# Kernel tuning notes

Hardware: AMD Instinct MI355X
Metric: run time of the kernel (lower is better)

## Reference

```python
import jax, jax.numpy as jnp
import numpy as np

N = 50000      # nodes
E = 800000     # edges (avg degree 16)
F_IN = 256
F_OUT = 128
ALPHA = 0.2    # leaky-relu negative slope


def setup_inputs() -> dict:
    key = jax.random.key(0)
    k1, k2, k3, k4 = jax.random.split(key, 4)
    x = jax.random.normal(k1, (N, F_IN), dtype=jnp.float32)
    # xavier_uniform-like scale for W (gain=1.414)
    limit_w = 1.414 * np.sqrt(6.0 / (F_IN + F_OUT))
    W = jax.random.uniform(k2, (F_IN, F_OUT), dtype=jnp.float32, minval=-limit_w, maxval=limit_w)
    limit_a = 1.414 * np.sqrt(6.0 / (2 * F_OUT + 1))
    a = jax.random.uniform(k3, (2 * F_OUT, 1), dtype=jnp.float32, minval=-limit_a, maxval=limit_a)
    edge = jax.random.randint(k4, (2, E), 0, N)  # edge[0]=row/src, edge[1]=col/dst
    return {"x": x, "W": W, "a": a, "edge": edge}


def reference(x, W, a, edge):
    h = x @ W                                   # [N, F_OUT]
    src, dst = edge[0], edge[1]                 # [E], [E]
    # cat([h_i, h_j], 1) @ a == h_i @ a[:F] + h_j @ a[F:] -> compute per-node halves once
    s_src = h @ a[:F_OUT, 0]                    # [N]
    s_dst = h @ a[F_OUT:, 0]                    # [N]
    e = jax.nn.leaky_relu(s_src[src] + s_dst[dst], negative_slope=ALPHA)  # [E]
    # segment softmax over edges grouped by row (dim=1 softmax of sparse [N,N])
    m = jax.ops.segment_max(e, src, num_segments=N)       # [N], -inf for empty rows
    ex = jnp.exp(e - m[src])                               # [E]
    denom = jax.ops.segment_sum(ex, src, num_segments=N)   # [N]
    attn = ex / denom[src]                                  # [E]
    # sparse mm: h_prime[i] = sum_{edges with row i} attn * h[dst]
    h_prime = jax.ops.segment_sum(attn[:, None] * h[dst], src, num_segments=N)  # [N, F_OUT]
    return jax.nn.elu(h_prime)                  # concat=True path
```

## Files before the change

### kernel.cpp

```cpp
#include <hip/hip_runtime.h>
#include <hip/hip_bf16.h>
#include <math.h>

#define F_IN   256
#define F_OUT  128
#define ALPHA  0.2f
#define TM     64

typedef __attribute__((ext_vector_type(8))) short s16x8;
typedef __attribute__((ext_vector_type(4))) float f32x4;

__device__ __forceinline__ ushort f2bf(float f) {
  __hip_bfloat16 h = __float2bfloat16(f);
  return *reinterpret_cast<ushort*>(&h);
}
__device__ __forceinline__ uint pk2bf(float lo, float hi) {
  return (uint)f2bf(lo) | ((uint)f2bf(hi) << 16);
}
__device__ __forceinline__ float bflo(uint u) { return __uint_as_float(u << 16); }
__device__ __forceinline__ float bfhi(uint u) { return __uint_as_float(u & 0xffff0000u); }

__global__ __launch_bounds__(256) void prep_kernel(
    const float* __restrict__ W, const float* __restrict__ avec,
    ushort* __restrict__ Wf, ushort* __restrict__ Wfs,
    int4* __restrict__ deg4, int n4, int ZB) {
  int b = blockIdx.x;
  if (b < ZB) {
    int i = b * 256 + threadIdx.x;
    if (i < n4) deg4[i] = make_int4(0, 0, 0, 0);
  } else if (b < ZB + 16) {
    int idx = (b - ZB) * 256 + threadIdx.x;
    int kb = idx >> 7, c = idx & 127;
    union { s16x8 v; ushort u[8]; } t;
#pragma unroll
    for (int j = 0; j < 8; ++j) t.u[j] = f2bf(W[(kb * 8 + j) * F_OUT + c]);
    *(s16x8*)&Wf[(size_t)idx * 8] = t.v;
  } else {
    int k = threadIdx.x;
    float s1 = 0.f, s2 = 0.f;
    for (int c = 0; c < F_OUT; ++c) {
      float wv = W[k * F_OUT + c];
      s1 += wv * avec[c];
      s2 += wv * avec[F_OUT + c];
    }
    int kb = k >> 3, j8 = k & 7;
    ushort b1 = f2bf(s1), b2 = f2bf(s2);
#pragma unroll
    for (int cc = 0; cc < 16; ++cc) {
      ushort v = (cc == 0) ? b1 : (cc == 1) ? b2 : (ushort)0;
      Wfs[((size_t)kb * 16 + cc) * 8 + j8] = v;
    }
  }
}

__global__ __launch_bounds__(256) void gemm_hist_kernel(
    const float* __restrict__ X, const ushort* __restrict__ Wf,
    const ushort* __restrict__ Wfs,
    uint* __restrict__ Hb32, float* __restrict__ s_src, float* __restrict__ s_dst,
    int M, int G,
    const int* __restrict__ src, int* __restrict__ deg,
    int* __restrict__ rank, int E) {
  __shared__ __align__(16) char Xs[4][8192];
  const int tid = threadIdx.x;

  if (blockIdx.x >= G) {
    int e0 = ((blockIdx.x - G) * 256 + tid) * 4;
    if (e0 + 4 <= E) {
      int4 s4 = *(const int4*)(src + e0);
      int4 r4;
      r4.x = atomicAdd(&deg[s4.x], 1);
      r4.y = atomicAdd(&deg[s4.y], 1);
      r4.z = atomicAdd(&deg[s4.z], 1);
      r4.w = atomicAdd(&deg[s4.w], 1);
      *(int4*)(rank + e0) = r4;
    } else {
      for (int e = e0; e < E; ++e) rank[e] = atomicAdd(&deg[src[e]], 1);
    }
    return;
  }

  const int l = tid & 63;
  const int w = tid >> 6;
  const int lc = l & 15;
  const int lg = l >> 4;
  const int rowW = blockIdx.x * TM + w * 16;
  char* myXs = Xs[w];

  const int h = l >> 5, kbs = l & 31;
#pragma unroll
  for (int i = 0; i < 8; ++i) {
    int rr = 2 * i + h;
    int gr = rowW + rr; gr = (gr < M) ? gr : (M - 1);
    const f32x4* p = (const f32x4*)(X + (size_t)gr * F_IN + kbs * 8);
    f32x4 v0 = p[0], v1 = p[1];
    union { s16x8 vv; ushort uu[8]; } t;
    t.uu[0] = f2bf(v0[0]); t.uu[1] = f2bf(v0[1]); t.uu[2] = f2bf(v0[2]); t.uu[3] = f2bf(v0[3]);
    t.uu[4] = f2bf(v1[0]); t.uu[5] = f2bf(v1[1]); t.uu[6] = f2bf(v1[2]); t.uu[7] = f2bf(v1[3]);
    int byte = kbs * 256 + (rr ^ (kbs & 7)) * 16;
    *(s16x8*)(myXs + byte) = t.vv;
  }

  f32x4 acc[8] = {};
  f32x4 aS = {0.f, 0.f, 0.f, 0.f};
#pragma unroll
  for (int ks = 0; ks < 8; ++ks) {
    int kb = ks * 4 + lg;
    int ab = kb * 256 + (lc ^ (kb & 7)) * 16;
    s16x8 af = *(const s16x8*)(myXs + ab);
    s16x8 bS = *(const s16x8*)&Wfs[((size_t)kb * 16 + lc) * 8];
#pragma unroll
    for (int j = 0; j < 8; ++j) {
      s16x8 bj = *(const s16x8*)&Wf[((size_t)kb * F_OUT + j * 16 + lc) * 8];
      acc[j] = __builtin_amdgcn_mfma_f32_16x16x32_bf16(af, bj, acc[j], 0, 0, 0);
    }
    aS = __builtin_amdgcn_mfma_f32_16x16x32_bf16(af, bS, aS, 0, 0, 0);
  }

#pragma unroll
  for (int q = 0; q < 4; ++q) {
    int rg = rowW + lg * 4 + q;
    if (rg < M) {
#pragma unroll
      for (int j = 0; j < 4; ++j)
        Hb32[(size_t)rg * 64 + j * 16 + lc] = pk2bf(acc[j][q], acc[j + 4][q]);
    }
  }

  if (lc < 2) {
    float* sout = (lc == 0) ? s_src : s_dst;
#pragma unroll
    for (int q = 0; q < 4; ++q) {
      int rg = rowW + lg * 4 + q;
      if (rg < M) sout[rg] = aS[q];
    }
  }
}

__global__ void block_sums_kernel(const int* __restrict__ deg, int* __restrict__ bs, int N) {
  int i = blockIdx.x * 256 + threadIdx.x;
  int v = (i < N) ? deg[i] : 0;
  int lane = threadIdx.x & 63, w = threadIdx.x >> 6;
#pragma unroll
  for (int d = 32; d >= 1; d >>= 1) v += __shfl_down(v, d);
  __shared__ int wsum[4];
  if (lane == 0) wsum[w] = v;
  __syncthreads();
  if (threadIdx.x == 0) bs[blockIdx.x] = wsum[0] + wsum[1] + wsum[2] + wsum[3];
}

__global__ void scan_deg_kernel(const int* __restrict__ deg, const int* __restrict__ bs,
                                int* __restrict__ rowptr, int N, int E, int NS) {
  __shared__ int sc[256];
  __shared__ int wsumA[4], wsumB[4];
  int tid = threadIdx.x;
  int lane = tid & 63, w = tid >> 6;

  int bv = (tid < NS) ? bs[tid] : 0;
  int ibv = bv;
#pragma unroll
  for (int d = 1; d < 64; d <<= 1) {
    int t = __shfl_up(ibv, d);
    if (lane >= d) ibv += t;
  }
  if (lane == 63) wsumA[w] = ibv;
  __syncthreads();
  int boff = 0;
  for (int x = 0; x < w; ++x) boff += wsumA[x];
  sc[tid] = boff + ibv - bv;

  int i = blockIdx.x * 256 + tid;
  int v = (i < N) ? deg[i] : 0;
  int iv = v;
#pragma unroll
  for (int d = 1; d < 64; d <<= 1) {
    int t = __shfl_up(iv, d);
    if (lane >= d) iv += t;
  }
  if (lane == 63) wsumB[w] = iv;
  __syncthreads();
  int off = sc[blockIdx.x];
  for (int x = 0; x < w; ++x) off += wsumB[x];
  int excl = off + iv - v;
  if (i < N) rowptr[i] = excl;
  if (i == N - 1) rowptr[N] = E;
}

__global__ __launch_bounds__(256) void scatter_kernel(
    const int* __restrict__ src, const int* __restrict__ dst,
    const int* __restrict__ rank, const int* __restrict__ rowptr,
    int* __restrict__ colidx, int E) {
  int e0 = (blockIdx.x * 256 + threadIdx.x) * 4;
  if (e0 + 4 <= E) {
    int4 s4 = *(const int4*)(src + e0);
    int4 d4 = *(const int4*)(dst + e0);
    int4 r4 = *(const int4*)(rank + e0);
    colidx[rowptr[s4.x] + r4.x] = d4.x;
    colidx[rowptr[s4.y] + r4.y] = d4.y;
    colidx[rowptr[s4.z] + r4.z] = d4.z;
    colidx[rowptr[s4.w] + r4.w] = d4.w;
  } else {
    for (int e = e0; e < E; ++e) colidx[rowptr[src[e]] + rank[e]] = dst[e];
  }
}

__global__ __launch_bounds__(256) void aggregate_kernel(
    const uint* __restrict__ H32, const float* __restrict__ s_src,
    const float* __restrict__ s_dst, const int* __restrict__ rowptr,
    const int* __restrict__ colidx, float* __restrict__ out, int M) {
  int node = blockIdx.x * 4 + (threadIdx.x >> 6);
  int l = threadIdx.x & 63;
  if (node >= M) return;
  const int g = l >> 4;
  const int lc = l & 15;
  int beg = rowptr[node], end = rowptr[node + 1];
  float ssrc = s_src[node];
  float m = -INFINITY, denom = 0.f;
  float acc[8] = {};

  for (int base = beg; base < end; base += 64) {
    int cnt = end - base; if (cnt > 64) cnt = 64;
    int jv = 0; float ev = -INFINITY;
    if (l < cnt) {
      jv = colidx[base + l];
      float e = ssrc + s_dst[jv];
      ev = (e > 0.f) ? e : ALPHA * e;
    }
    float cm = ev;
#pragma unroll
    for (int mask = 1; mask < 64; mask <<= 1) cm = fmaxf(cm, __shfl_xor(cm, mask));
    float mn = fmaxf(m, cm);
    float wv = (l < cnt) ? __expf(ev - mn) : 0.f;
    float sw = wv;
#pragma unroll
    for (int mask = 1; mask < 64; mask <<= 1) sw += __shfl_xor(sw, mask);
    float resc = __expf(m - mn);
    denom = denom * resc + sw;
#pragma unroll
    for (int t = 0; t < 8; ++t) acc[t] *= resc;
    m = mn;

    for (int k = 0; k < cnt; k += 8) {
      int k0 = k + g, k1 = k + 4 + g;
      int j0 = __shfl(jv, k0);
      int j1 = (k1 < 64) ? __shfl(jv, k1) : 0;
      float w0 = __shfl(wv, k0);
      float w1 = (k1 < 64) ? __shfl(wv, k1) : 0.f;
      uint4 u0 = *(const uint4*)(H32 + ((size_t)(uint)j0 << 6) + lc * 4);
      uint4 u1 = *(const uint4*)(H32 + ((size_t)(uint)j1 << 6) + lc * 4);
      acc[0] += w0 * bflo(u0.x) + w1 * bflo(u1.x);
      acc[1] += w0 * bfhi(u0.x) + w1 * bfhi(u1.x);
      acc[2] += w0 * bflo(u0.y) + w1 * bflo(u1.y);
      acc[3] += w0 * bfhi(u0.y) + w1 * bfhi(u1.y);
      acc[4] += w0 * bflo(u0.z) + w1 * bflo(u1.z);
      acc[5] += w0 * bfhi(u0.z) + w1 * bfhi(u1.z);
      acc[6] += w0 * bflo(u0.w) + w1 * bflo(u1.w);
      acc[7] += w0 * bfhi(u0.w) + w1 * bfhi(u1.w);
    }
  }

#pragma unroll
  for (int t = 0; t < 8; ++t) {
    acc[t] += __shfl_xor(acc[t], 16);
    acc[t] += __shfl_xor(acc[t], 32);
  }
  float inv = (denom > 0.f) ? 1.f / denom : 0.f;
  if (g == 0) {
    float4 v;
    v.x = acc[0] * inv; v.y = acc[2] * inv; v.z = acc[4] * inv; v.w = acc[6] * inv;
    v.x = (v.x > 0.f) ? v.x : __expf(v.x) - 1.f;
    v.y = (v.y > 0.f) ? v.y : __expf(v.y) - 1.f;
    v.z = (v.z > 0.f) ? v.z : __expf(v.z) - 1.f;
    v.w = (v.w > 0.f) ? v.w : __expf(v.w) - 1.f;
    *(float4*)&out[(size_t)node * 128 + lc * 4] = v;
  } else if (g == 1) {
    float4 v;
    v.x = acc[1] * inv; v.y = acc[3] * inv; v.z = acc[5] * inv; v.w = acc[7] * inv;
    v.x = (v.x > 0.f) ? v.x : __expf(v.x) - 1.f;
    v.y = (v.y > 0.f) ? v.y : __expf(v.y) - 1.f;
    v.z = (v.z > 0.f) ? v.z : __expf(v.z) - 1.f;
    v.w = (v.w > 0.f) ? v.w : __expf(v.w) - 1.f;
    *(float4*)&out[(size_t)node * 128 + 64 + lc * 4] = v;
  }
}

extern "C" void kernel_launch(void* const* d_in, const int* in_sizes, int n_in,
                              void* d_out, int out_size, void* d_ws, size_t ws_size,
                              hipStream_t stream) {
  const float* x    = (const float*)d_in[0];
  const float* W    = (const float*)d_in[1];
  const float* avec = (const float*)d_in[2];
  const int*   edge = (const int*)d_in[3];

  const int M = in_sizes[0] / F_IN;
  const int E = in_sizes[3] / 2;
  const int* src = edge;
  const int* dst = edge + E;
  float* out = (float*)d_out;

  char* ws = (char*)d_ws;
  uint*   Hb32  = (uint*)ws;   ws += (size_t)M * 64 * sizeof(uint);
  ushort* Wf    = (ushort*)ws; ws += (size_t)32 * F_OUT * 8 * sizeof(ushort);
  ushort* Wfs   = (ushort*)ws; ws += (size_t)32 * 16 * 8 * sizeof(ushort);
  float* s_src  = (float*)ws;  ws += (size_t)M * sizeof(float);
  float* s_dst  = (float*)ws;  ws += (size_t)M * sizeof(float);
  int*   deg    = (int*)ws;    ws += (size_t)M * sizeof(int);
  int*   rowptr = (int*)ws;    ws += (size_t)(M + 1) * sizeof(int);
  int*   rank   = (int*)ws;    ws += (size_t)E * sizeof(int);
  int*   colidx = (int*)ws;    ws += (size_t)E * sizeof(int);
  int*   bsums  = (int*)ws;

  const int NS = (M + 255) / 256;
  const int n4 = M / 4;
  const int ZB = (n4 + 255) / 256;
  const int E4 = (E + 1023) / 1024;
  const int G  = (M + TM - 1) / TM;

  prep_kernel<<<ZB + 17, 256, 0, stream>>>(W, avec, Wf, Wfs, (int4*)deg, n4, ZB);
  gemm_hist_kernel<<<G + E4, 256, 0, stream>>>(x, Wf, Wfs, Hb32, s_src, s_dst,
                                               M, G, src, deg, rank, E);
  block_sums_kernel<<<NS, 256, 0, stream>>>(deg, bsums, M);
  scan_deg_kernel<<<NS, 256, 0, stream>>>(deg, bsums, rowptr, M, E, NS);
  scatter_kernel<<<E4, 256, 0, stream>>>(src, dst, rank, rowptr, colidx, E);
  aggregate_kernel<<<(M + 3) / 4, 256, 0, stream>>>(Hb32, s_src, s_dst, rowptr, colidx, out, M);
}
```

Baseline: 108.3 us.

## Fuse degree scan into one kernel and batch X loads in GEMM

Result: slower. 113.3 us (+4.7%).

```diff
diff --git a/kernel.cpp b/kernel.cpp
--- a/kernel.cpp
+++ b/kernel.cpp
@@ -53,7 +53,7 @@
   }
 }
 
-__global__ __launch_bounds__(256) void gemm_hist_kernel(
+__global__ __launch_bounds__(256, 2) void gemm_hist_kernel(
     const float* __restrict__ X, const ushort* __restrict__ Wf,
     const ushort* __restrict__ Wfs,
     uint* __restrict__ Hb32, float* __restrict__ s_src, float* __restrict__ s_dst,
@@ -87,12 +87,19 @@
   char* myXs = Xs[w];
 
   const int h = l >> 5, kbs = l & 31;
+  f32x4 v[16];
+#pragma unroll
+  for (int i = 0; i < 8; ++i) {
+    int gr = rowW + 2 * i + h;
+    gr = (gr < M) ? gr : (M - 1);
+    const f32x4* p = (const f32x4*)(X + (size_t)gr * F_IN + kbs * 8);
+    v[2 * i]     = p[0];
+    v[2 * i + 1] = p[1];
+  }
 #pragma unroll
   for (int i = 0; i < 8; ++i) {
     int rr = 2 * i + h;
-    int gr = rowW + rr; gr = (gr < M) ? gr : (M - 1);
-    const f32x4* p = (const f32x4*)(X + (size_t)gr * F_IN + kbs * 8);
-    f32x4 v0 = p[0], v1 = p[1];
+    f32x4 v0 = v[2 * i], v1 = v[2 * i + 1];
     union { s16x8 vv; ushort uu[8]; } t;
     t.uu[0] = f2bf(v0[0]); t.uu[1] = f2bf(v0[1]); t.uu[2] = f2bf(v0[2]); t.uu[3] = f2bf(v0[3]);
     t.uu[4] = f2bf(v1[0]); t.uu[5] = f2bf(v1[1]); t.uu[6] = f2bf(v1[2]); t.uu[7] = f2bf(v1[3]);
@@ -136,39 +143,26 @@
   }
 }
 
-__global__ void block_sums_kernel(const int* __restrict__ deg, int* __restrict__ bs, int N) {
-  int i = blockIdx.x * 256 + threadIdx.x;
-  int v = (i < N) ? deg[i] : 0;
-  int lane = threadIdx.x & 63, w = threadIdx.x >> 6;
-#pragma unroll
-  for (int d = 32; d >= 1; d >>= 1) v += __shfl_down(v, d);
-  __shared__ int wsum[4];
-  if (lane == 0) wsum[w] = v;
+__global__ __launch_bounds__(256) void scan_fused_kernel(
+    const int* __restrict__ deg, int* __restrict__ rowptr, int N, int E) {
+  __shared__ int wsumA[4], wsumB[4];
+  const int b = blockIdx.x, tid = threadIdx.x;
+  const int lane = tid & 63, w = tid >> 6;
+
+  const int4* d4 = (const int4*)deg;
+  int n4 = b * 64;
+  int s = 0;
+  for (int i = tid; i < n4; i += 256) {
+    int4 vv = d4[i];
+    s += vv.x + vv.y + vv.z + vv.w;
+  }
+#pragma unroll
+  for (int d = 32; d >= 1; d >>= 1) s += __shfl_down(s, d);
+  if (lane == 0) wsumA[w] = s;
   __syncthreads();
-  if (threadIdx.x == 0) bs[blockIdx.x] = wsum[0] + wsum[1] + wsum[2] + wsum[3];
-}
-
-__global__ void scan_deg_kernel(const int* __restrict__ deg, const int* __restrict__ bs,
-                                int* __restrict__ rowptr, int N, int E, int NS) {
-  __shared__ int sc[256];
-  __shared__ int wsumA[4], wsumB[4];
-  int tid = threadIdx.x;
-  int lane = tid & 63, w = tid >> 6;
-
-  int bv = (tid < NS) ? bs[tid] : 0;
-  int ibv = bv;
-#pragma unroll
-  for (int d = 1; d < 64; d <<= 1) {
-    int t = __shfl_up(ibv, d);
-    if (lane >= d) ibv += t;
-  }
-  if (lane == 63) wsumA[w] = ibv;
-  __syncthreads();
-  int boff = 0;
-  for (int x = 0; x < w; ++x) boff += wsumA[x];
-  sc[tid] = boff + ibv - bv;
-
-  int i = blockIdx.x * 256 + tid;
+  int base = wsumA[0] + wsumA[1] + wsumA[2] + wsumA[3];
+
+  int i = b * 256 + tid;
   int v = (i < N) ? deg[i] : 0;
   int iv = v;
 #pragma unroll
@@ -178,7 +172,7 @@
   }
   if (lane == 63) wsumB[w] = iv;
   __syncthreads();
-  int off = sc[blockIdx.x];
+  int off = base;
   for (int x = 0; x < w; ++x) off += wsumB[x];
   int excl = off + iv - v;
   if (i < N) rowptr[i] = excl;
@@ -307,7 +301,6 @@
   int*   rowptr = (int*)ws;    ws += (size_t)(M + 1) * sizeof(int);
   int*   rank   = (int*)ws;    ws += (size_t)E * sizeof(int);
   int*   colidx = (int*)ws;    ws += (size_t)E * sizeof(int);
-  int*   bsums  = (int*)ws;
 
   const int NS = (M + 255) / 256;
   const int n4 = M / 4;
@@ -318,8 +311,7 @@
   prep_kernel<<<ZB + 17, 256, 0, stream>>>(W, avec, Wf, Wfs, (int4*)deg, n4, ZB);
   gemm_hist_kernel<<<G + E4, 256, 0, stream>>>(x, Wf, Wfs, Hb32, s_src, s_dst,
                                                M, G, src, deg, rank, E);
-  block_sums_kernel<<<NS, 256, 0, stream>>>(deg, bsums, M);
-  scan_deg_kernel<<<NS, 256, 0, stream>>>(deg, bsums, rowptr, M, E, NS);
+  scan_fused_kernel<<<NS, 256, 0, stream>>>(deg, rowptr, M, E);
   scatter_kernel<<<E4, 256, 0, stream>>>(src, dst, rank, rowptr, colidx, E);
   aggregate_kernel<<<(M + 3) / 4, 256, 0, stream>>>(Hb32, s_src, s_dst, rowptr, colidx, out, M);
 }
```
